# Kernel optimization log

Measured on AMD Instinct MI355X. Metric: run time of the kernel, lower is better.

The kernel has to match this reference:

```python
import jax, jax.numpy as jnp
import numpy as np

B, T, E, A = 4, 4096, 1024, 1024

def setup_inputs() -> dict:
    key = jax.random.key(0)
    k1, k2, k3, k4 = jax.random.split(key, 4)
    scale = 1.0 / np.sqrt(E)  # ~ nn.Linear default init scale
    return {
        "embedded": jax.random.normal(k1, (B, T, E), dtype=jnp.float32),
        "Wq": jax.random.uniform(k2, (A, E), jnp.float32, -scale, scale),
        "Wk": jax.random.uniform(k3, (A, E), jnp.float32, -scale, scale),
        "Wv": jax.random.uniform(k4, (A, E), jnp.float32, -scale, scale),
    }

def reference(embedded, Wq, Wk, Wv):
    # QKV projections (nn.Linear without bias: x @ W.T)
    q = jnp.einsum('bte,ae->bta', embedded, Wq)
    k = jnp.einsum('bte,ae->bta', embedded, Wk)
    v = jnp.einsum('bte,ae->bta', embedded, Wv)
    A_dim = q.shape[-1]
    # scaled scores [B, T, T]
    scores = jnp.einsum('bqa,bka->bqk', q, k) / jnp.sqrt(jnp.float32(A_dim))
    # causal mask (lower triangular allowed)
    Tq = scores.shape[-1]
    causal = jnp.tril(jnp.ones((Tq, Tq), dtype=bool))
    scores = jnp.where(causal, scores, -jnp.inf)
    probs = jax.nn.softmax(scores, axis=-1)
    out = jnp.einsum('bqk,bka->bqa', probs, v)
    return jnp.round(out, 4)
```

## Files before the change

kernel.cpp:

```cpp
#include <hip/hip_runtime.h>
#include <hip/hip_bf16.h>

using bf16 = __hip_bfloat16;

typedef __attribute__((ext_vector_type(4))) float f32x4;
typedef __attribute__((ext_vector_type(8))) short short8;

typedef const void __attribute__((address_space(1)))* gas1_t;
typedef void __attribute__((address_space(3)))* las3_t;
#define GLDS(gp, lp) __builtin_amdgcn_global_load_lds((gas1_t)(gp), (las3_t)(lp), 16, 0, 0)

__device__ inline short f2bfbits(float f) {
  union { bf16 h; short s; } u;
  u.h = __float2bfloat16(f);
  return u.s;
}
__device__ inline float bf2f(short u) {
  unsigned x = ((unsigned)(unsigned short)u) << 16;
  float f; __builtin_memcpy(&f, &x, 4); return f;
}

__device__ inline void store_out(float* C, size_t idx, float v) { C[idx] = v; }
__device__ inline void store_out(bf16* C, size_t idx, float v) { C[idx] = __float2bfloat16(v); }

template<typename TOUT, int MODE>
__global__ __launch_bounds__(512, 2) void gemm256(
    const short* __restrict__ A, int lda, size_t sAz,
    const short* __restrict__ B, int ldb, size_t sBz,
    TOUT* __restrict__ C, int ldc, size_t sCz,
    int K, float scale)
{
  int bx, by;
  if constexpr (MODE == 1) {
    const int i = blockIdx.x;
    by = (int)((__builtin_sqrtf(8.f * (float)i + 1.f) - 1.f) * 0.5f);
    if (((by * (by + 1)) >> 1) > i) by--;
    else if ((((by + 1) * (by + 2)) >> 1) <= i) by++;
    bx = i - ((by * (by + 1)) >> 1);
  } else {
    bx = blockIdx.x; by = blockIdx.y;
  }
  const int z = blockIdx.z;
  const int tri_by = (by * (by + 1)) >> 1;

  A += (size_t)z * sAz;
  B += (size_t)z * sBz;
  C += (size_t)z * sCz;

  int Klen = K;
  if (MODE == 2) Klen = min(K, (by + 1) * 256);
  const int NT = Klen >> 5;

  __shared__ short As[3][256 * 32];
  __shared__ short Bs[3][256 * 32];

  const int t = threadIdx.x;
  const int lane = t & 63;
  const int wave = t >> 6;
  const int wm = wave >> 2;
  const int wn = wave & 3;
  const int fr = lane & 15, kh = lane >> 4;
  const int koff = ((kh ^ ((fr >> 1) & 3)) << 3);

  int srow[2], scol[2];
  #pragma unroll
  for (int j = 0; j < 2; j++) {
    int e = j * 512 + t;
    srow[j] = e >> 2;
    scol[j] = (((e & 3) ^ ((e >> 3) & 3)) << 3);
  }

  f32x4 acc[8][4];
  #pragma unroll
  for (int i = 0; i < 8; i++)
    #pragma unroll
    for (int j = 0; j < 4; j++) acc[i][j] = (f32x4){0.f, 0.f, 0.f, 0.f};

  auto STAGE_A = [&](int kt) {
    const int buf = kt % 3, k0 = kt * 32;
    #pragma unroll
    for (int j = 0; j < 2; j++) {
      const short* pa;
      if constexpr (MODE == 2)
        pa = A + (size_t)(tri_by + (k0 >> 8)) * 65536 + (size_t)srow[j] * 256 + (k0 & 255) + scol[j];
      else
        pa = A + (size_t)(by * 256 + srow[j]) * lda + k0 + scol[j];
      GLDS(pa, (char*)&As[buf][0] + j * 8192 + wave * 1024);
    }
  };
  auto STAGE_B = [&](int kt) {
    const int buf = kt % 3, k0 = kt * 32;
    #pragma unroll
    for (int j = 0; j < 2; j++) {
      const short* pb = B + (size_t)(bx * 256 + srow[j]) * ldb + k0 + scol[j];
      GLDS(pb, (char*)&Bs[buf][0] + j * 8192 + wave * 1024);
    }
  };

  STAGE_A(0); STAGE_B(0);
  STAGE_A(1); STAGE_B(1);
  asm volatile("s_waitcnt vmcnt(4)\ns_barrier" ::: "memory");

  const int arow = wm * 128 + fr;
  const int brow = wn * 64 + fr;

  for (int kt = 0; kt < NT; kt++) {
    const short* as = &As[kt % 3][0];
    const short* bs = &Bs[kt % 3][0];
    short8 af[4], bfr[4];

    #pragma unroll
    for (int n = 0; n < 4; n++) bfr[n] = *(const short8*)&bs[(brow + n * 16) * 32 + koff];
    #pragma unroll
    for (int m = 0; m < 4; m++) af[m] = *(const short8*)&as[(arow + m * 16) * 32 + koff];
    if (kt + 2 < NT) STAGE_A(kt + 2);
    __builtin_amdgcn_s_barrier();
    asm volatile("s_waitcnt lgkmcnt(0)" ::: "memory");
    __builtin_amdgcn_sched_barrier(0);
    __builtin_amdgcn_s_setprio(1);
    #pragma unroll
    for (int m = 0; m < 4; m++)
      #pragma unroll
      for (int n = 0; n < 4; n++)
        acc[m][n] = __builtin_amdgcn_mfma_f32_16x16x32_bf16(af[m], bfr[n], acc[m][n], 0, 0, 0);
    __builtin_amdgcn_s_setprio(0);
    __builtin_amdgcn_sched_barrier(0);

    #pragma unroll
    for (int m = 0; m < 4; m++) af[m] = *(const short8*)&as[(arow + (m + 4) * 16) * 32 + koff];
    if (kt + 2 < NT) STAGE_B(kt + 2);
    __builtin_amdgcn_s_barrier();
    asm volatile("s_waitcnt lgkmcnt(0)" ::: "memory");
    __builtin_amdgcn_sched_barrier(0);
    __builtin_amdgcn_s_setprio(1);
    #pragma unroll
    for (int m = 0; m < 4; m++)
      #pragma unroll
      for (int n = 0; n < 4; n++)
        acc[m + 4][n] = __builtin_amdgcn_mfma_f32_16x16x32_bf16(af[m], bfr[n], acc[m + 4][n], 0, 0, 0);
    __builtin_amdgcn_s_setprio(0);
    __builtin_amdgcn_sched_barrier(0);

    if (kt + 2 < NT)      asm volatile("s_waitcnt vmcnt(4)\ns_barrier" ::: "memory");
    else if (kt + 1 < NT) asm volatile("s_waitcnt vmcnt(0)\ns_barrier" ::: "memory");
  }

  #pragma unroll
  for (int m = 0; m < 8; m++)
    #pragma unroll
    for (int n = 0; n < 4; n++) {
      int col_l = wn * 64 + n * 16 + fr;
      #pragma unroll
      for (int r = 0; r < 4; r++) {
        int row_l = wm * 128 + m * 16 + kh * 4 + r;
        if constexpr (MODE == 1)
          store_out(C, (size_t)(tri_by + bx) * 65536 + (size_t)row_l * 256 + col_l,
                    acc[m][n][r] * scale);
        else
          store_out(C, (size_t)(by * 256 + row_l) * ldc + bx * 256 + col_l,
                    acc[m][n][r] * scale);
      }
    }
}

__global__ __launch_bounds__(256) void cvt_bf16(
    const float* __restrict__ in, bf16* __restrict__ out, int n, float scale)
{
  for (int i = (blockIdx.x * 256 + threadIdx.x) * 8; i < n; i += gridDim.x * 2048) {
    f32x4 v0 = *(const f32x4*)&in[i];
    f32x4 v1 = *(const f32x4*)&in[i + 4];
    short8 o = { f2bfbits(v0[0] * scale), f2bfbits(v0[1] * scale),
                 f2bfbits(v0[2] * scale), f2bfbits(v0[3] * scale),
                 f2bfbits(v1[0] * scale), f2bfbits(v1[1] * scale),
                 f2bfbits(v1[2] * scale), f2bfbits(v1[3] * scale) };
    *(short8*)&out[i] = o;
  }
}

__global__ __launch_bounds__(256) void softmax_causal_packed(short* SP, int T)
{
  __shared__ float rowv[4096];
  __shared__ float red[4];
  const int r = blockIdx.x;
  const int z = blockIdx.y;
  const int rb = r >> 8, rl = r & 255;
  const size_t tri = (size_t)((rb * (rb + 1)) >> 1);
  short* base = SP + (size_t)z * 136 * 65536;
  const int L = r + 1;
  const int kend = (rb + 1) * 256;
  const int t = threadIdx.x;

  float lmax = -3.0e38f;
  for (int i = t * 8; i < kend; i += 2048) {
    short8 s = *(const short8*)(base + (tri + (i >> 8)) * 65536 + (size_t)rl * 256 + (i & 255));
    #pragma unroll
    for (int j = 0; j < 8; j++) {
      float v = bf2f(s[j]);
      rowv[i + j] = v;
      if (i + j < L) lmax = fmaxf(lmax, v);
    }
  }
  #pragma unroll
  for (int o = 32; o > 0; o >>= 1) lmax = fmaxf(lmax, __shfl_down(lmax, o));
  if ((t & 63) == 0) red[t >> 6] = lmax;
  __syncthreads();
  const float m = fmaxf(fmaxf(red[0], red[1]), fmaxf(red[2], red[3]));
  __syncthreads();

  float lsum = 0.f;
  for (int i = t; i < kend; i += 256) {
    float e = (i < L) ? __expf(rowv[i] - m) : 0.f;
    rowv[i] = e;
    lsum += e;
  }
  #pragma unroll
  for (int o = 32; o > 0; o >>= 1) lsum += __shfl_down(lsum, o);
  if ((t & 63) == 0) red[t >> 6] = lsum;
  __syncthreads();
  const float inv = 1.f / (red[0] + red[1] + red[2] + red[3]);

  for (int i = t * 8; i < kend; i += 2048) {
    short8 o;
    #pragma unroll
    for (int j = 0; j < 8; j++) o[j] = f2bfbits(rowv[i + j] * inv);
    *(short8*)(base + (tri + (i >> 8)) * 65536 + (size_t)rl * 256 + (i & 255)) = o;
  }
}

extern "C" void kernel_launch(void* const* d_in, const int* in_sizes, int n_in,
                              void* d_out, int out_size, void* d_ws, size_t ws_size,
                              hipStream_t stream) {
  (void)in_sizes; (void)n_in; (void)out_size; (void)ws_size;
  const float* X  = (const float*)d_in[0];
  const float* Wq = (const float*)d_in[1];
  const float* Wk = (const float*)d_in[2];
  const float* Wv = (const float*)d_in[3];
  float* Out = (float*)d_out;

  const int Bn = 4, T = 4096, E = 1024, Ad = 1024;
  const int M = Bn * T;

  char* ws = (char*)d_ws;
  short* QKb = (short*)ws;
  short* Vt  = (short*)(ws + 67108864);
  short* Xb  = (short*)(ws + 100663296);
  short* Wqk = (short*)(ws + 134217728);
  short* Wvb = (short*)(ws + 138412032);
  short* SP  = (short*)(ws + 100663296);

  dim3 blk(256), blk5(512);
  const float qscale = 0.03125f;
  const size_t SPz = (size_t)136 * 65536;

  cvt_bf16<<<dim3(8192), blk, 0, stream>>>(X, (bf16*)Xb, M * E, 1.0f);
  cvt_bf16<<<dim3(512),  blk, 0, stream>>>(Wq, (bf16*)Wqk, Ad * E, qscale);
  cvt_bf16<<<dim3(512),  blk, 0, stream>>>(Wk, (bf16*)(Wqk + (size_t)Ad * E), Ad * E, 1.0f);
  cvt_bf16<<<dim3(512),  blk, 0, stream>>>(Wv, (bf16*)Wvb, Ad * E, 1.0f);

  gemm256<bf16, 0><<<dim3(2048 / 256, M / 256), blk5, 0, stream>>>(
      Xb, E, 0, Wqk, E, 0, (bf16*)QKb, 2048, 0, E, 1.0f);
  gemm256<bf16, 0><<<dim3(M / 256, Ad / 256), blk5, 0, stream>>>(
      Wvb, E, 0, Xb, E, 0, (bf16*)Vt, M, 0, E, 1.0f);

  gemm256<bf16, 1><<<dim3(136, 1, Bn), blk5, 0, stream>>>(
      QKb, 2048, (size_t)T * 2048,
      QKb + 1024, 2048, (size_t)T * 2048,
      (bf16*)SP, 256, SPz, Ad, 1.0f);

  softmax_causal_packed<<<dim3(T, Bn), blk, 0, stream>>>(SP, T);

  gemm256<float, 2><<<dim3(Ad / 256, T / 256, Bn), blk5, 0, stream>>>(
      SP, 256, SPz,
      Vt, M, (size_t)T,
      Out, Ad, (size_t)T * Ad, T, 1.0f);
}
```

Before: 399.2 us.

## Make GEMMs persistent with XCC-local atomic tile queues and work stealing

Turns the four GEMM launches into persistent kernels. Each workgroup reads its XCC id and pulls tiles from a per-XCC atomic counter queue, stealing from other XCCs' queues once its own is empty. Tile orderings are arranged so tiles that share operands land on the same XCC for L2 reuse, and the causal PV GEMM pairs long and short rows to balance load. This adds an atomic and a barrier per tile plus a memset of the counters, and launches grids sized to fit in one wave of occupancy.

```diff
diff --git a/kernel.cpp b/kernel.cpp
--- a/kernel.cpp
+++ b/kernel.cpp
@@ -28,31 +28,17 @@
     const short* __restrict__ A, int lda, size_t sAz,
     const short* __restrict__ B, int ldb, size_t sBz,
     TOUT* __restrict__ C, int ldc, size_t sCz,
-    int K, float scale)
+    int K, float scale, int* __restrict__ qctr)
 {
-  int bx, by;
-  if constexpr (MODE == 1) {
-    const int i = blockIdx.x;
-    by = (int)((__builtin_sqrtf(8.f * (float)i + 1.f) - 1.f) * 0.5f);
-    if (((by * (by + 1)) >> 1) > i) by--;
-    else if ((((by + 1) * (by + 2)) >> 1) <= i) by++;
-    bx = i - ((by * (by + 1)) >> 1);
-  } else {
-    bx = blockIdx.x; by = blockIdx.y;
-  }
-  const int z = blockIdx.z;
-  const int tri_by = (by * (by + 1)) >> 1;
-
-  A += (size_t)z * sAz;
-  B += (size_t)z * sBz;
-  C += (size_t)z * sCz;
-
-  int Klen = K;
-  if (MODE == 2) Klen = min(K, (by + 1) * 256);
-  const int NT = Klen >> 5;
+  constexpr int QSZ = (MODE == 0) ? 64 : (MODE == 1) ? 68 : 32;
 
   __shared__ short As[3][256 * 32];
   __shared__ short Bs[3][256 * 32];
+  __shared__ int s_tile;
+
+  int xcc;
+  asm volatile("s_getreg_b32 %0, hwreg(HW_REG_XCC_ID)" : "=s"(xcc));
+  xcc &= 7;
 
   const int t = threadIdx.x;
   const int lane = t & 63;
@@ -69,98 +55,145 @@
     srow[j] = e >> 2;
     scol[j] = (((e & 3) ^ ((e >> 3) & 3)) << 3);
   }
-
-  f32x4 acc[8][4];
-  #pragma unroll
-  for (int i = 0; i < 8; i++)
-    #pragma unroll
-    for (int j = 0; j < 4; j++) acc[i][j] = (f32x4){0.f, 0.f, 0.f, 0.f};
-
-  auto STAGE_A = [&](int kt) {
-    const int buf = kt % 3, k0 = kt * 32;
-    #pragma unroll
-    for (int j = 0; j < 2; j++) {
-      const short* pa;
-      if constexpr (MODE == 2)
-        pa = A + (size_t)(tri_by + (k0 >> 8)) * 65536 + (size_t)srow[j] * 256 + (k0 & 255) + scol[j];
-      else
-        pa = A + (size_t)(by * 256 + srow[j]) * lda + k0 + scol[j];
-      GLDS(pa, (char*)&As[buf][0] + j * 8192 + wave * 1024);
-    }
-  };
-  auto STAGE_B = [&](int kt) {
-    const int buf = kt % 3, k0 = kt * 32;
-    #pragma unroll
-    for (int j = 0; j < 2; j++) {
-      const short* pb = B + (size_t)(bx * 256 + srow[j]) * ldb + k0 + scol[j];
-      GLDS(pb, (char*)&Bs[buf][0] + j * 8192 + wave * 1024);
-    }
-  };
-
-  STAGE_A(0); STAGE_B(0);
-  STAGE_A(1); STAGE_B(1);
-  asm volatile("s_waitcnt vmcnt(4)\ns_barrier" ::: "memory");
-
   const int arow = wm * 128 + fr;
   const int brow = wn * 64 + fr;
 
-  for (int kt = 0; kt < NT; kt++) {
-    const short* as = &As[kt % 3][0];
-    const short* bs = &Bs[kt % 3][0];
-    short8 af[4], bfr[4];
-
+  for (;;) {
+    if (t == 0) {
+      int tile = -1;
+      #pragma unroll
+      for (int k = 0; k < 8; k++) {
+        int q = (xcc + k) & 7;
+        int v = atomicAdd(&qctr[q], 1);
+        if (v < QSZ) { tile = q * QSZ + v; break; }
+      }
+      s_tile = tile;
+    }
+    __syncthreads();
+    const int tile = s_tile;
+    if (tile < 0) return;
+
+    int bx, by, z;
+    if constexpr (MODE == 0) {
+      const int q = tile / QSZ, v = tile % QSZ;
+      by = q * 8 + (v >> 3); bx = v & 7; z = 0;
+    } else if constexpr (MODE == 1) {
+      z = tile / 136;
+      const int r = tile % 136;
+      by = (int)((__builtin_sqrtf(8.f * (float)r + 1.f) - 1.f) * 0.5f);
+      if (((by * (by + 1)) >> 1) > r) by--;
+      else if ((((by + 1) * (by + 2)) >> 1) <= r) by++;
+      bx = r - ((by * (by + 1)) >> 1);
+    } else if constexpr (MODE == 2) {
+      z = tile >> 6;
+      const int s = tile & 63, pr = s >> 3, k = s & 7;
+      by = (k < 4) ? pr : 15 - pr;
+      bx = k & 3;
+    } else {
+      const int q = tile / QSZ, v = tile % QSZ;
+      bx = q * 8 + (v >> 2); by = v & 3; z = 0;
+    }
+    const int tri_by = (by * (by + 1)) >> 1;
+
+    const short* Az = A + (size_t)z * sAz;
+    const short* Bz = B + (size_t)z * sBz;
+    TOUT* Cz = C + (size_t)z * sCz;
+
+    int Klen = K;
+    if (MODE == 2) Klen = min(K, (by + 1) * 256);
+    const int NT = Klen >> 5;
+
+    f32x4 acc[8][4];
     #pragma unroll
-    for (int n = 0; n < 4; n++) bfr[n] = *(const short8*)&bs[(brow + n * 16) * 32 + koff];
+    for (int i = 0; i < 8; i++)
+      #pragma unroll
+      for (int j = 0; j < 4; j++) acc[i][j] = (f32x4){0.f, 0.f, 0.f, 0.f};
+
+    auto STAGE_A = [&](int kt) {
+      const int buf = kt % 3, k0 = kt * 32;
+      #pragma unroll
+      for (int j = 0; j < 2; j++) {
+        const short* pa;
+        if constexpr (MODE == 2)
+          pa = Az + (size_t)(tri_by + (k0 >> 8)) * 65536 + (size_t)srow[j] * 256 + (k0 & 255) + scol[j];
+        else
+          pa = Az + (size_t)(by * 256 + srow[j]) * lda + k0 + scol[j];
+        GLDS(pa, (char*)&As[buf][0] + j * 8192 + wave * 1024);
+      }
+    };
+    auto STAGE_B = [&](int kt) {
+      const int buf = kt % 3, k0 = kt * 32;
+      #pragma unroll
+      for (int j = 0; j < 2; j++) {
+        const short* pb = Bz + (size_t)(bx * 256 + srow[j]) * ldb + k0 + scol[j];
+        GLDS(pb, (char*)&Bs[buf][0] + j * 8192 + wave * 1024);
+      }
+    };
+
+    STAGE_A(0); STAGE_B(0);
+    STAGE_A(1); STAGE_B(1);
+    asm volatile("s_waitcnt vmcnt(4)\ns_barrier" ::: "memory");
+
+    for (int kt = 0; kt < NT; kt++) {
+      const short* as = &As[kt % 3][0];
+      const short* bs = &Bs[kt % 3][0];
+      short8 af[4], bfr[4];
+
+      #pragma unroll
+      for (int n = 0; n < 4; n++) bfr[n] = *(const short8*)&bs[(brow + n * 16) * 32 + koff];
+      #pragma unroll
+      for (int m = 0; m < 4; m++) af[m] = *(const short8*)&as[(arow + m * 16) * 32 + koff];
+      if (kt + 2 < NT) STAGE_A(kt + 2);
+      __builtin_amdgcn_s_barrier();
+      asm volatile("s_waitcnt lgkmcnt(0)" ::: "memory");
+      __builtin_amdgcn_sched_barrier(0);
+      __builtin_amdgcn_s_setprio(1);
+      #pragma unroll
+      for (int m = 0; m < 4; m++)
+        #pragma unroll
+        for (int n = 0; n < 4; n++)
+          acc[m][n] = __builtin_amdgcn_mfma_f32_16x16x32_bf16(af[m], bfr[n], acc[m][n], 0, 0, 0);
+      __builtin_amdgcn_s_setprio(0);
+      __builtin_amdgcn_sched_barrier(0);
+
+      #pragma unroll
+      for (int m = 0; m < 4; m++) af[m] = *(const short8*)&as[(arow + (m + 4) * 16) * 32 + koff];
+      if (kt + 2 < NT) STAGE_B(kt + 2);
+      __builtin_amdgcn_s_barrier();
+      asm volatile("s_waitcnt lgkmcnt(0)" ::: "memory");
+      __builtin_amdgcn_sched_barrier(0);
+      __builtin_amdgcn_s_setprio(1);
+      #pragma unroll
+      for (int m = 0; m < 4; m++)
+        #pragma unroll
+        for (int n = 0; n < 4; n++)
+          acc[m + 4][n] = __builtin_amdgcn_mfma_f32_16x16x32_bf16(af[m], bfr[n], acc[m + 4][n], 0, 0, 0);
+      __builtin_amdgcn_s_setprio(0);
+      __builtin_amdgcn_sched_barrier(0);
+
+      if (kt + 2 < NT)      asm volatile("s_waitcnt vmcnt(4)\ns_barrier" ::: "memory");
+      else if (kt + 1 < NT) asm volatile("s_waitcnt vmcnt(0)\ns_barrier" ::: "memory");
+    }
+
     #pragma unroll
-    for (int m = 0; m < 4; m++) af[m] = *(const short8*)&as[(arow + m * 16) * 32 + koff];
-    if (kt + 2 < NT) STAGE_A(kt + 2);
-    __builtin_amdgcn_s_barrier();
-    asm volatile("s_waitcnt lgkmcnt(0)" ::: "memory");
-    __builtin_amdgcn_sched_barrier(0);
-    __builtin_amdgcn_s_setprio(1);
-    #pragma unroll
-    for (int m = 0; m < 4; m++)
-      #pragma unroll
-      for (int n = 0; n < 4; n++)
-        acc[m][n] = __builtin_amdgcn_mfma_f32_16x16x32_bf16(af[m], bfr[n], acc[m][n], 0, 0, 0);
-    __builtin_amdgcn_s_setprio(0);
-    __builtin_amdgcn_sched_barrier(0);
-
-    #pragma unroll
-    for (int m = 0; m < 4; m++) af[m] = *(const short8*)&as[(arow + (m + 4) * 16) * 32 + koff];
-    if (kt + 2 < NT) STAGE_B(kt + 2);
-    __builtin_amdgcn_s_barrier();
-    asm volatile("s_waitcnt lgkmcnt(0)" ::: "memory");
-    __builtin_amdgcn_sched_barrier(0);
-    __builtin_amdgcn_s_setprio(1);
-    #pragma unroll
-    for (int m = 0; m < 4; m++)
-      #pragma unroll
-      for (int n = 0; n < 4; n++)
-        acc[m + 4][n] = __builtin_amdgcn_mfma_f32_16x16x32_bf16(af[m], bfr[n], acc[m + 4][n], 0, 0, 0);
-    __builtin_amdgcn_s_setprio(0);
-    __builtin_amdgcn_sched_barrier(0);
-
-    if (kt + 2 < NT)      asm volatile("s_waitcnt vmcnt(4)\ns_barrier" ::: "memory");
-    else if (kt + 1 < NT) asm volatile("s_waitcnt vmcnt(0)\ns_barrier" ::: "memory");
-  }
-
-  #pragma unroll
-  for (int m = 0; m < 8; m++)
-    #pragma unroll
-    for (int n = 0; n < 4; n++) {
-      int col_l = wn * 64 + n * 16 + fr;
-      #pragma unroll
-      for (int r = 0; r < 4; r++) {
-        int row_l = wm * 128 + m * 16 + kh * 4 + r;
-        if constexpr (MODE == 1)
-          store_out(C, (size_t)(tri_by + bx) * 65536 + (size_t)row_l * 256 + col_l,
-                    acc[m][n][r] * scale);
-        else
-          store_out(C, (size_t)(by * 256 + row_l) * ldc + bx * 256 + col_l,
-                    acc[m][n][r] * scale);
+    for (int m = 0; m < 8; m++)
+      #pragma unroll
+      for (int n = 0; n < 4; n++) {
+        int col_l = wn * 64 + n * 16 + fr;
+        #pragma unroll
+        for (int r = 0; r < 4; r++) {
+          int row_l = wm * 128 + m * 16 + kh * 4 + r;
+          if constexpr (MODE == 1)
+            store_out(Cz, (size_t)(tri_by + bx) * 65536 + (size_t)row_l * 256 + col_l,
+                      acc[m][n][r] * scale);
+          else
+            store_out(Cz, (size_t)(by * 256 + row_l) * ldc + bx * 256 + col_l,
+                      acc[m][n][r] * scale);
+        }
       }
-    }
+
+    __syncthreads();
+  }
 }
 
 __global__ __launch_bounds__(256) void cvt_bf16(
@@ -247,30 +280,33 @@
   short* Wqk = (short*)(ws + 134217728);
   short* Wvb = (short*)(ws + 138412032);
   short* SP  = (short*)(ws + 100663296);
+  int*  qctr = (int*)(ws + 188743680);
 
   dim3 blk(256), blk5(512);
   const float qscale = 0.03125f;
   const size_t SPz = (size_t)136 * 65536;
+
+  hipMemsetAsync(qctr, 0, 4 * 16 * sizeof(int), stream);
 
   cvt_bf16<<<dim3(8192), blk, 0, stream>>>(X, (bf16*)Xb, M * E, 1.0f);
   cvt_bf16<<<dim3(512),  blk, 0, stream>>>(Wq, (bf16*)Wqk, Ad * E, qscale);
   cvt_bf16<<<dim3(512),  blk, 0, stream>>>(Wk, (bf16*)(Wqk + (size_t)Ad * E), Ad * E, 1.0f);
   cvt_bf16<<<dim3(512),  blk, 0, stream>>>(Wv, (bf16*)Wvb, Ad * E, 1.0f);
 
-  gemm256<bf16, 0><<<dim3(2048 / 256, M / 256), blk5, 0, stream>>>(
-      Xb, E, 0, Wqk, E, 0, (bf16*)QKb, 2048, 0, E, 1.0f);
-  gemm256<bf16, 0><<<dim3(M / 256, Ad / 256), blk5, 0, stream>>>(
-      Wvb, E, 0, Xb, E, 0, (bf16*)Vt, M, 0, E, 1.0f);
-
-  gemm256<bf16, 1><<<dim3(136, 1, Bn), blk5, 0, stream>>>(
+  gemm256<bf16, 0><<<dim3(512), blk5, 0, stream>>>(
+      Xb, E, 0, Wqk, E, 0, (bf16*)QKb, 2048, 0, E, 1.0f, qctr + 0);
+  gemm256<bf16, 3><<<dim3(256), blk5, 0, stream>>>(
+      Wvb, E, 0, Xb, E, 0, (bf16*)Vt, M, 0, E, 1.0f, qctr + 16);
+
+  gemm256<bf16, 1><<<dim3(544), blk5, 0, stream>>>(
       QKb, 2048, (size_t)T * 2048,
       QKb + 1024, 2048, (size_t)T * 2048,
-      (bf16*)SP, 256, SPz, Ad, 1.0f);
+      (bf16*)SP, 256, SPz, Ad, 1.0f, qctr + 32);
 
   softmax_causal_packed<<<dim3(T, Bn), blk, 0, stream>>>(SP, T);
 
-  gemm256<float, 2><<<dim3(Ad / 256, T / 256, Bn), blk5, 0, stream>>>(
+  gemm256<float, 2><<<dim3(256), blk5, 0, stream>>>(
       SP, 256, SPz,
       Vt, M, (size_t)T,
-      Out, Ad, (size_t)T * Ad, T, 1.0f);
-}
+      Out, Ad, (size_t)T * Ad, T, 1.0f, qctr + 48);
+}
```

Measured after the change: 484.7 us. +21.4%, slower.

## Switch GEMMs to 128x256 tiles with BK=64 four-slot pipeline and balanced scheduling

Applied to the files above, without the earlier changes.

The 256x256 GEMM tile becomes a 128x256 tile, giving twice as many blocks and a 16-accumulator-per-wave footprint. The K loop now covers 64 per iteration, split into two 32-wide halves, using a four-slot LDS ring with prefetch issued between the halves. The causal PV GEMM uses a flattened grid that pairs short and long row-blocks across batches to balance triangular work, and the score GEMM maps the packed triangle onto half-height tiles. This aims at better occupancy and load balance, at the cost of more redundant B-tile loads per output and more complex index math.

```diff
diff --git a/kernel.cpp b/kernel.cpp
--- a/kernel.cpp
+++ b/kernel.cpp
@@ -24,35 +24,46 @@
 __device__ inline void store_out(bf16* C, size_t idx, float v) { C[idx] = __float2bfloat16(v); }
 
 template<typename TOUT, int MODE>
-__global__ __launch_bounds__(512, 2) void gemm256(
+__global__ __launch_bounds__(512, 2) void gemm8p(
     const short* __restrict__ A, int lda, size_t sAz,
     const short* __restrict__ B, int ldb, size_t sBz,
     TOUT* __restrict__ C, int ldc, size_t sCz,
     int K, float scale)
 {
-  int bx, by;
+  int bx, by, z;
   if constexpr (MODE == 1) {
     const int i = blockIdx.x;
-    by = (int)((__builtin_sqrtf(8.f * (float)i + 1.f) - 1.f) * 0.5f);
-    if (((by * (by + 1)) >> 1) > i) by--;
-    else if ((((by + 1) * (by + 2)) >> 1) <= i) by++;
-    bx = i - ((by * (by + 1)) >> 1);
+    int u = (int)((__builtin_sqrtf(4.f * (float)i + 1.f) - 1.f) * 0.5f);
+    while (u > 0 && u * (u + 1) > i) u--;
+    while ((u + 1) * (u + 2) <= i) u++;
+    const int rem = i - u * (u + 1);
+    if (rem < u + 1) { by = 2 * u; bx = rem; }
+    else             { by = 2 * u + 1; bx = rem - (u + 1); }
+    z = blockIdx.z;
+  } else if constexpr (MODE == 2) {
+    const int w = blockIdx.x;
+    const int k = w >> 8, c = w & 255;
+    bx = c & 3;
+    const int h = c >> 2;
+    const int byb = h & 31, zb = h >> 5;
+    by = k ? 31 - byb : byb;
+    z = zb + 2 * k;
   } else {
-    bx = blockIdx.x; by = blockIdx.y;
-  }
-  const int z = blockIdx.z;
-  const int tri_by = (by * (by + 1)) >> 1;
-
-  A += (size_t)z * sAz;
-  B += (size_t)z * sBz;
-  C += (size_t)z * sCz;
+    bx = blockIdx.x; by = blockIdx.y; z = 0;
+  }
+  const int u_rb = by >> 1;
+  const int tri_u = (u_rb * (u_rb + 1)) >> 1;
+
+  const short* Az = A + (size_t)z * sAz;
+  const short* Bz = B + (size_t)z * sBz;
+  TOUT* Cz = C + (size_t)z * sCz;
 
   int Klen = K;
-  if (MODE == 2) Klen = min(K, (by + 1) * 256);
-  const int NT = Klen >> 5;
-
-  __shared__ short As[3][256 * 32];
-  __shared__ short Bs[3][256 * 32];
+  if (MODE == 2) Klen = min(K, (u_rb + 1) * 256);
+  const int NT = Klen >> 6;
+
+  __shared__ short As[4][128 * 32];
+  __shared__ short Bs[4][256 * 32];
 
   const int t = threadIdx.x;
   const int lane = t & 63;
@@ -62,59 +73,64 @@
   const int fr = lane & 15, kh = lane >> 4;
   const int koff = ((kh ^ ((fr >> 1) & 3)) << 3);
 
-  int srow[2], scol[2];
-  #pragma unroll
-  for (int j = 0; j < 2; j++) {
-    int e = j * 512 + t;
-    srow[j] = e >> 2;
-    scol[j] = (((e & 3) ^ ((e >> 3) & 3)) << 3);
-  }
-
-  f32x4 acc[8][4];
-  #pragma unroll
-  for (int i = 0; i < 8; i++)
+  const int aro = (wm * 64 + fr) * 32;
+  const int bro = (wn * 64 + fr) * 32;
+  const int abase = by * 128;
+  const int bbase = bx * 256;
+
+  const int s_row = t >> 2;
+  const int s_sc = (((t & 3) ^ ((s_row >> 1) & 3)) << 3);
+
+  f32x4 acc[4][4];
+  #pragma unroll
+  for (int i = 0; i < 4; i++)
     #pragma unroll
     for (int j = 0; j < 4; j++) acc[i][j] = (f32x4){0.f, 0.f, 0.f, 0.f};
 
-  auto STAGE_A = [&](int kt) {
-    const int buf = kt % 3, k0 = kt * 32;
+  auto STAGE_A = [&](int kt, int ks) {
+    const int slot = (2 * kt + ks) & 3;
+    const int k0 = kt * 64 + ks * 32;
+    const short* pa;
+    if constexpr (MODE == 2)
+      pa = Az + (size_t)(tri_u + (k0 >> 8)) * 65536
+              + (size_t)((by & 1) * 128 + s_row) * 256 + (k0 & 255) + s_sc;
+    else
+      pa = Az + (size_t)(abase + s_row) * lda + k0 + s_sc;
+    GLDS(pa, (char*)&As[slot][0] + t * 16);
+  };
+  auto STAGE_B = [&](int kt, int ks) {
+    const int slot = (2 * kt + ks) & 3;
+    const int k0 = kt * 64 + ks * 32;
     #pragma unroll
     for (int j = 0; j < 2; j++) {
-      const short* pa;
-      if constexpr (MODE == 2)
-        pa = A + (size_t)(tri_by + (k0 >> 8)) * 65536 + (size_t)srow[j] * 256 + (k0 & 255) + scol[j];
-      else
-        pa = A + (size_t)(by * 256 + srow[j]) * lda + k0 + scol[j];
-      GLDS(pa, (char*)&As[buf][0] + j * 8192 + wave * 1024);
+      const int e = j * 512 + t;
+      const int row = e >> 2;
+      const int sc = (((e & 3) ^ ((row >> 1) & 3)) << 3);
+      const short* pb = Bz + (size_t)(bbase + row) * ldb + k0 + sc;
+      GLDS(pb, (char*)&Bs[slot][0] + j * 8192 + t * 16);
     }
   };
-  auto STAGE_B = [&](int kt) {
-    const int buf = kt % 3, k0 = kt * 32;
-    #pragma unroll
-    for (int j = 0; j < 2; j++) {
-      const short* pb = B + (size_t)(bx * 256 + srow[j]) * ldb + k0 + scol[j];
-      GLDS(pb, (char*)&Bs[buf][0] + j * 8192 + wave * 1024);
-    }
-  };
-
-  STAGE_A(0); STAGE_B(0);
-  STAGE_A(1); STAGE_B(1);
-  asm volatile("s_waitcnt vmcnt(4)\ns_barrier" ::: "memory");
-
-  const int arow = wm * 128 + fr;
-  const int brow = wn * 64 + fr;
+
+  STAGE_A(0, 0); STAGE_B(0, 0);
+  STAGE_A(0, 1); STAGE_B(0, 1);
+  STAGE_A(1, 0); STAGE_B(1, 0);
+  STAGE_A(1, 1); STAGE_B(1, 1);
 
   for (int kt = 0; kt < NT; kt++) {
-    const short* as = &As[kt % 3][0];
-    const short* bs = &Bs[kt % 3][0];
-    short8 af[4], bfr[4];
-
-    #pragma unroll
-    for (int n = 0; n < 4; n++) bfr[n] = *(const short8*)&bs[(brow + n * 16) * 32 + koff];
-    #pragma unroll
-    for (int m = 0; m < 4; m++) af[m] = *(const short8*)&as[(arow + m * 16) * 32 + koff];
-    if (kt + 2 < NT) STAGE_A(kt + 2);
+    const short* as0 = &As[(2 * kt) & 3][0];
+    const short* bs0 = &Bs[(2 * kt) & 3][0];
+    const short* as1 = &As[(2 * kt + 1) & 3][0];
+    const short* bs1 = &Bs[(2 * kt + 1) & 3][0];
+    short8 af[4], bf[4];
+
+    if (kt >= 1 && kt + 1 < NT) { STAGE_A(kt + 1, 1); STAGE_B(kt + 1, 1); }
+    if (kt == NT - 1) asm volatile("s_waitcnt vmcnt(0)" ::: "memory");
+    else              asm volatile("s_waitcnt vmcnt(6)" ::: "memory");
     __builtin_amdgcn_s_barrier();
+    #pragma unroll
+    for (int n = 0; n < 4; n++) bf[n] = *(const short8*)&bs0[bro + n * 512 + koff];
+    #pragma unroll
+    for (int m = 0; m < 4; m++) af[m] = *(const short8*)&as0[aro + m * 512 + koff];
     asm volatile("s_waitcnt lgkmcnt(0)" ::: "memory");
     __builtin_amdgcn_sched_barrier(0);
     __builtin_amdgcn_s_setprio(1);
@@ -122,14 +138,15 @@
     for (int m = 0; m < 4; m++)
       #pragma unroll
       for (int n = 0; n < 4; n++)
-        acc[m][n] = __builtin_amdgcn_mfma_f32_16x16x32_bf16(af[m], bfr[n], acc[m][n], 0, 0, 0);
+        acc[m][n] = __builtin_amdgcn_mfma_f32_16x16x32_bf16(af[m], bf[n], acc[m][n], 0, 0, 0);
     __builtin_amdgcn_s_setprio(0);
-    __builtin_amdgcn_sched_barrier(0);
-
-    #pragma unroll
-    for (int m = 0; m < 4; m++) af[m] = *(const short8*)&as[(arow + (m + 4) * 16) * 32 + koff];
-    if (kt + 2 < NT) STAGE_B(kt + 2);
+
     __builtin_amdgcn_s_barrier();
+    if (kt + 2 < NT) { STAGE_A(kt + 2, 0); STAGE_B(kt + 2, 0); }
+    #pragma unroll
+    for (int n = 0; n < 4; n++) bf[n] = *(const short8*)&bs1[bro + n * 512 + koff];
+    #pragma unroll
+    for (int m = 0; m < 4; m++) af[m] = *(const short8*)&as1[aro + m * 512 + koff];
     asm volatile("s_waitcnt lgkmcnt(0)" ::: "memory");
     __builtin_amdgcn_sched_barrier(0);
     __builtin_amdgcn_s_setprio(1);
@@ -137,27 +154,25 @@
     for (int m = 0; m < 4; m++)
       #pragma unroll
       for (int n = 0; n < 4; n++)
-        acc[m + 4][n] = __builtin_amdgcn_mfma_f32_16x16x32_bf16(af[m], bfr[n], acc[m + 4][n], 0, 0, 0);
+        acc[m][n] = __builtin_amdgcn_mfma_f32_16x16x32_bf16(af[m], bf[n], acc[m][n], 0, 0, 0);
     __builtin_amdgcn_s_setprio(0);
-    __builtin_amdgcn_sched_barrier(0);
-
-    if (kt + 2 < NT)      asm volatile("s_waitcnt vmcnt(4)\ns_barrier" ::: "memory");
-    else if (kt + 1 < NT) asm volatile("s_waitcnt vmcnt(0)\ns_barrier" ::: "memory");
-  }
-
-  #pragma unroll
-  for (int m = 0; m < 8; m++)
+    __builtin_amdgcn_s_barrier();
+  }
+
+  #pragma unroll
+  for (int m = 0; m < 4; m++)
     #pragma unroll
     for (int n = 0; n < 4; n++) {
       int col_l = wn * 64 + n * 16 + fr;
       #pragma unroll
       for (int r = 0; r < 4; r++) {
-        int row_l = wm * 128 + m * 16 + kh * 4 + r;
+        int row_l = wm * 64 + m * 16 + kh * 4 + r;
         if constexpr (MODE == 1)
-          store_out(C, (size_t)(tri_by + bx) * 65536 + (size_t)row_l * 256 + col_l,
+          store_out(Cz, (size_t)(tri_u + bx) * 65536
+                        + (size_t)((by & 1) * 128 + row_l) * 256 + col_l,
                     acc[m][n][r] * scale);
         else
-          store_out(C, (size_t)(by * 256 + row_l) * ldc + bx * 256 + col_l,
+          store_out(Cz, (size_t)(by * 128 + row_l) * ldc + bx * 256 + col_l,
                     acc[m][n][r] * scale);
       }
     }
@@ -257,19 +272,19 @@
   cvt_bf16<<<dim3(512),  blk, 0, stream>>>(Wk, (bf16*)(Wqk + (size_t)Ad * E), Ad * E, 1.0f);
   cvt_bf16<<<dim3(512),  blk, 0, stream>>>(Wv, (bf16*)Wvb, Ad * E, 1.0f);
 
-  gemm256<bf16, 0><<<dim3(2048 / 256, M / 256), blk5, 0, stream>>>(
+  gemm8p<bf16, 0><<<dim3(2048 / 256, M / 128), blk5, 0, stream>>>(
       Xb, E, 0, Wqk, E, 0, (bf16*)QKb, 2048, 0, E, 1.0f);
-  gemm256<bf16, 0><<<dim3(M / 256, Ad / 256), blk5, 0, stream>>>(
+  gemm8p<bf16, 0><<<dim3(M / 256, Ad / 128), blk5, 0, stream>>>(
       Wvb, E, 0, Xb, E, 0, (bf16*)Vt, M, 0, E, 1.0f);
 
-  gemm256<bf16, 1><<<dim3(136, 1, Bn), blk5, 0, stream>>>(
+  gemm8p<bf16, 1><<<dim3(272, 1, Bn), blk5, 0, stream>>>(
       QKb, 2048, (size_t)T * 2048,
       QKb + 1024, 2048, (size_t)T * 2048,
       (bf16*)SP, 256, SPz, Ad, 1.0f);
 
   softmax_causal_packed<<<dim3(T, Bn), blk, 0, stream>>>(SP, T);
 
-  gemm256<float, 2><<<dim3(Ad / 256, T / 256, Bn), blk5, 0, stream>>>(
+  gemm8p<float, 2><<<dim3(512), blk5, 0, stream>>>(
       SP, 256, SPz,
       Vt, M, (size_t)T,
       Out, Ad, (size_t)T * Ad, T, 1.0f);
```

Result: slower. 528.3 us (+32.3%).

## Restructure GEMM pipeline to 64-wide K stages and add dedicated causal PV kernel

Applied to the files above, without the earlier changes.

Changes the main 256x256 GEMM from a triple-buffered 32-wide K loop to a double-buffered 64-wide K step split into two halves. Loads are issued per half-stage across four sub-iterations, the LDS XOR swizzle is removed, and the occupancy hint of two blocks per SM is dropped. The PV product moves to a new 128x128-tile kernel with a grid ordered to balance causal work (pairing short and long row blocks) and a simple synchronous load loop. The risks are LDS bank conflicts without the swizzle, lower occupancy, and an unpipelined PV kernel.

```diff
diff --git a/kernel.cpp b/kernel.cpp
--- a/kernel.cpp
+++ b/kernel.cpp
@@ -24,7 +24,7 @@
 __device__ inline void store_out(bf16* C, size_t idx, float v) { C[idx] = __float2bfloat16(v); }
 
 template<typename TOUT, int MODE>
-__global__ __launch_bounds__(512, 2) void gemm256(
+__global__ __launch_bounds__(512) void gemm8(
     const short* __restrict__ A, int lda, size_t sAz,
     const short* __restrict__ B, int ldb, size_t sBz,
     TOUT* __restrict__ C, int ldc, size_t sCz,
@@ -47,12 +47,10 @@
   B += (size_t)z * sBz;
   C += (size_t)z * sCz;
 
-  int Klen = K;
-  if (MODE == 2) Klen = min(K, (by + 1) * 256);
-  const int NT = Klen >> 5;
-
-  __shared__ short As[3][256 * 32];
-  __shared__ short Bs[3][256 * 32];
+  const int NT = K >> 6;
+
+  __shared__ short AS[2][2][8192];
+  __shared__ short BS[2][2][8192];
 
   const int t = threadIdx.x;
   const int lane = t & 63;
@@ -60,15 +58,6 @@
   const int wm = wave >> 2;
   const int wn = wave & 3;
   const int fr = lane & 15, kh = lane >> 4;
-  const int koff = ((kh ^ ((fr >> 1) & 3)) << 3);
-
-  int srow[2], scol[2];
-  #pragma unroll
-  for (int j = 0; j < 2; j++) {
-    int e = j * 512 + t;
-    srow[j] = e >> 2;
-    scol[j] = (((e & 3) ^ ((e >> 3) & 3)) << 3);
-  }
 
   f32x4 acc[8][4];
   #pragma unroll
@@ -76,89 +65,164 @@
     #pragma unroll
     for (int j = 0; j < 4; j++) acc[i][j] = (f32x4){0.f, 0.f, 0.f, 0.f};
 
-  auto STAGE_A = [&](int kt) {
-    const int buf = kt % 3, k0 = kt * 32;
+  auto STAGE_A = [&](int tau, int h) {
+    if (tau >= NT) return;
+    const short* src = A + (size_t)(by * 256) * lda + tau * 64 + h * 32;
+    char* dst = (char*)&AS[tau & 1][h][0] + wave * 1024;
     #pragma unroll
     for (int j = 0; j < 2; j++) {
-      const short* pa;
-      if constexpr (MODE == 2)
-        pa = A + (size_t)(tri_by + (k0 >> 8)) * 65536 + (size_t)srow[j] * 256 + (k0 & 255) + scol[j];
-      else
-        pa = A + (size_t)(by * 256 + srow[j]) * lda + k0 + scol[j];
-      GLDS(pa, (char*)&As[buf][0] + j * 8192 + wave * 1024);
+      int e = j * 512 + t;
+      GLDS(src + (size_t)(e >> 2) * lda + (e & 3) * 8, dst + j * 8192);
     }
   };
-  auto STAGE_B = [&](int kt) {
-    const int buf = kt % 3, k0 = kt * 32;
+  auto STAGE_B = [&](int tau, int h) {
+    if (tau >= NT) return;
+    const short* src = B + (size_t)(bx * 256) * ldb + tau * 64 + h * 32;
+    char* dst = (char*)&BS[tau & 1][h][0] + wave * 1024;
     #pragma unroll
     for (int j = 0; j < 2; j++) {
-      const short* pb = B + (size_t)(bx * 256 + srow[j]) * ldb + k0 + scol[j];
-      GLDS(pb, (char*)&Bs[buf][0] + j * 8192 + wave * 1024);
+      int e = j * 512 + t;
+      GLDS(src + (size_t)(e >> 2) * ldb + (e & 3) * 8, dst + j * 8192);
     }
   };
 
-  STAGE_A(0); STAGE_B(0);
-  STAGE_A(1); STAGE_B(1);
-  asm volatile("s_waitcnt vmcnt(4)\ns_barrier" ::: "memory");
-
-  const int arow = wm * 128 + fr;
-  const int brow = wn * 64 + fr;
-
-  for (int kt = 0; kt < NT; kt++) {
-    const short* as = &As[kt % 3][0];
-    const short* bs = &Bs[kt % 3][0];
+  STAGE_A(0, 0); STAGE_B(0, 0);
+  STAGE_A(0, 1); STAGE_B(0, 1);
+  STAGE_A(1, 0); STAGE_B(1, 0);
+  asm volatile("s_waitcnt vmcnt(8)" ::: "memory");
+  __builtin_amdgcn_s_barrier();
+  __builtin_amdgcn_sched_barrier(0);
+
+  for (int s = 0; s < NT; s++) {
+    const int buf = s & 1;
+    #pragma unroll
+    for (int r = 0; r < 4; r++) {
+      const int kh2 = r >> 1, mh = r & 1;
+      short8 af[4], bfr[4];
+      #pragma unroll
+      for (int n = 0; n < 4; n++)
+        bfr[n] = *(const short8*)&BS[buf][kh2][(wn * 64 + n * 16 + fr) * 32 + kh * 8];
+      #pragma unroll
+      for (int m2 = 0; m2 < 4; m2++)
+        af[m2] = *(const short8*)&AS[buf][kh2][(wm * 128 + mh * 64 + m2 * 16 + fr) * 32 + kh * 8];
+
+      if      (r == 0) STAGE_A(s + 1, 1);
+      else if (r == 1) STAGE_B(s + 1, 1);
+      else if (r == 2) STAGE_A(s + 2, 0);
+      else             STAGE_B(s + 2, 0);
+
+      __builtin_amdgcn_s_barrier();
+      asm volatile("s_waitcnt lgkmcnt(0)" ::: "memory");
+      __builtin_amdgcn_sched_barrier(0);
+      __builtin_amdgcn_s_setprio(1);
+      #pragma unroll
+      for (int m2 = 0; m2 < 4; m2++)
+        #pragma unroll
+        for (int n = 0; n < 4; n++)
+          acc[mh * 4 + m2][n] =
+              __builtin_amdgcn_mfma_f32_16x16x32_bf16(af[m2], bfr[n], acc[mh * 4 + m2][n], 0, 0, 0);
+      __builtin_amdgcn_s_setprio(0);
+      __builtin_amdgcn_sched_barrier(0);
+
+      if (r == 1) {
+        if (s + 1 < NT) asm volatile("s_waitcnt vmcnt(8)" ::: "memory");
+        else            asm volatile("s_waitcnt vmcnt(0)" ::: "memory");
+      } else if (r == 3) {
+        if (s + 2 < NT) asm volatile("s_waitcnt vmcnt(8)" ::: "memory");
+        else            asm volatile("s_waitcnt vmcnt(0)" ::: "memory");
+      }
+      __builtin_amdgcn_s_barrier();
+      __builtin_amdgcn_sched_barrier(0);
+    }
+  }
+
+  #pragma unroll
+  for (int m = 0; m < 8; m++)
+    #pragma unroll
+    for (int n = 0; n < 4; n++) {
+      int col_l = wn * 64 + n * 16 + fr;
+      #pragma unroll
+      for (int r_ = 0; r_ < 4; r_++) {
+        int row_l = wm * 128 + m * 16 + kh * 4 + r_;
+        if constexpr (MODE == 1)
+          store_out(C, (size_t)(tri_by + bx) * 65536 + (size_t)row_l * 256 + col_l,
+                    acc[m][n][r_] * scale);
+        else
+          store_out(C, (size_t)(by * 256 + row_l) * ldc + bx * 256 + col_l,
+                    acc[m][n][r_] * scale);
+      }
+    }
+}
+
+__global__ __launch_bounds__(256) void gemm_pv(
+    const short* __restrict__ SP, const short* __restrict__ Vt,
+    float* __restrict__ Out)
+{
+  const int w = blockIdx.x;
+  const int c = w & 255, k = w >> 8;
+  const int bx = c & 7;
+  const int g = c >> 3;
+  const int by = (k & 1) ? 31 - g : g;
+  const int z = ((k & 1) << 1) | (k >> 1);
+
+  const int u = by >> 1;
+  const int tri_u = (u * (u + 1)) >> 1;
+  const short* A = SP + (size_t)z * 136 * 65536;
+  const int Klen = (u + 1) * 256;
+
+  __shared__ short a_lds[128 * 32];
+  __shared__ short b_lds[128 * 32];
+
+  const int t = threadIdx.x;
+  const int lane = t & 63;
+  const int wave = t >> 6;
+  const int wm = wave >> 1, wn = wave & 1;
+  const int fr = lane & 15, kh = lane >> 4;
+
+  f32x4 acc[4][4];
+  #pragma unroll
+  for (int i = 0; i < 4; i++)
+    #pragma unroll
+    for (int j = 0; j < 4; j++) acc[i][j] = (f32x4){0.f, 0.f, 0.f, 0.f};
+
+  for (int k0 = 0; k0 < Klen; k0 += 32) {
+    #pragma unroll
+    for (int i = 0; i < 2; i++) {
+      int e = i * 256 + t;
+      int r_ = e >> 2, c_ = (e & 3) * 8;
+      const short* pa = A + (size_t)(tri_u + (k0 >> 8)) * 65536
+                          + (size_t)((by & 1) * 128 + r_) * 256 + (k0 & 255) + c_;
+      const short* pb = Vt + (size_t)(bx * 128 + r_) * 16384 + z * 4096 + k0 + c_;
+      GLDS(pa, (char*)a_lds + i * 4096 + wave * 1024);
+      GLDS(pb, (char*)b_lds + i * 4096 + wave * 1024);
+    }
+    __syncthreads();
+
     short8 af[4], bfr[4];
-
-    #pragma unroll
-    for (int n = 0; n < 4; n++) bfr[n] = *(const short8*)&bs[(brow + n * 16) * 32 + koff];
-    #pragma unroll
-    for (int m = 0; m < 4; m++) af[m] = *(const short8*)&as[(arow + m * 16) * 32 + koff];
-    if (kt + 2 < NT) STAGE_A(kt + 2);
-    __builtin_amdgcn_s_barrier();
-    asm volatile("s_waitcnt lgkmcnt(0)" ::: "memory");
-    __builtin_amdgcn_sched_barrier(0);
-    __builtin_amdgcn_s_setprio(1);
+    #pragma unroll
+    for (int m = 0; m < 4; m++)
+      af[m] = *(const short8*)&a_lds[(wm * 64 + m * 16 + fr) * 32 + kh * 8];
+    #pragma unroll
+    for (int n = 0; n < 4; n++)
+      bfr[n] = *(const short8*)&b_lds[(wn * 64 + n * 16 + fr) * 32 + kh * 8];
     #pragma unroll
     for (int m = 0; m < 4; m++)
       #pragma unroll
       for (int n = 0; n < 4; n++)
         acc[m][n] = __builtin_amdgcn_mfma_f32_16x16x32_bf16(af[m], bfr[n], acc[m][n], 0, 0, 0);
-    __builtin_amdgcn_s_setprio(0);
-    __builtin_amdgcn_sched_barrier(0);
-
-    #pragma unroll
-    for (int m = 0; m < 4; m++) af[m] = *(const short8*)&as[(arow + (m + 4) * 16) * 32 + koff];
-    if (kt + 2 < NT) STAGE_B(kt + 2);
-    __builtin_amdgcn_s_barrier();
-    asm volatile("s_waitcnt lgkmcnt(0)" ::: "memory");
-    __builtin_amdgcn_sched_barrier(0);
-    __builtin_amdgcn_s_setprio(1);
-    #pragma unroll
-    for (int m = 0; m < 4; m++)
-      #pragma unroll
-      for (int n = 0; n < 4; n++)
-        acc[m + 4][n] = __builtin_amdgcn_mfma_f32_16x16x32_bf16(af[m], bfr[n], acc[m + 4][n], 0, 0, 0);
-    __builtin_amdgcn_s_setprio(0);
-    __builtin_amdgcn_sched_barrier(0);
-
-    if (kt + 2 < NT)      asm volatile("s_waitcnt vmcnt(4)\ns_barrier" ::: "memory");
-    else if (kt + 1 < NT) asm volatile("s_waitcnt vmcnt(0)\ns_barrier" ::: "memory");
-  }
-
-  #pragma unroll
-  for (int m = 0; m < 8; m++)
+    __syncthreads();
+  }
+
+  float* Cz = Out + (size_t)z * 4096 * 1024;
+  #pragma unroll
+  for (int m = 0; m < 4; m++)
     #pragma unroll
     for (int n = 0; n < 4; n++) {
       int col_l = wn * 64 + n * 16 + fr;
       #pragma unroll
-      for (int r = 0; r < 4; r++) {
-        int row_l = wm * 128 + m * 16 + kh * 4 + r;
-        if constexpr (MODE == 1)
-          store_out(C, (size_t)(tri_by + bx) * 65536 + (size_t)row_l * 256 + col_l,
-                    acc[m][n][r] * scale);
-        else
-          store_out(C, (size_t)(by * 256 + row_l) * ldc + bx * 256 + col_l,
-                    acc[m][n][r] * scale);
+      for (int r_ = 0; r_ < 4; r_++) {
+        int row_l = wm * 64 + m * 16 + kh * 4 + r_;
+        Cz[(size_t)(by * 128 + row_l) * 1024 + bx * 128 + col_l] = acc[m][n][r_];
       }
     }
 }
@@ -257,20 +321,17 @@
   cvt_bf16<<<dim3(512),  blk, 0, stream>>>(Wk, (bf16*)(Wqk + (size_t)Ad * E), Ad * E, 1.0f);
   cvt_bf16<<<dim3(512),  blk, 0, stream>>>(Wv, (bf16*)Wvb, Ad * E, 1.0f);
 
-  gemm256<bf16, 0><<<dim3(2048 / 256, M / 256), blk5, 0, stream>>>(
+  gemm8<bf16, 0><<<dim3(2048 / 256, M / 256), blk5, 0, stream>>>(
       Xb, E, 0, Wqk, E, 0, (bf16*)QKb, 2048, 0, E, 1.0f);
-  gemm256<bf16, 0><<<dim3(M / 256, Ad / 256), blk5, 0, stream>>>(
+  gemm8<bf16, 0><<<dim3(M / 256, Ad / 256), blk5, 0, stream>>>(
       Wvb, E, 0, Xb, E, 0, (bf16*)Vt, M, 0, E, 1.0f);
 
-  gemm256<bf16, 1><<<dim3(136, 1, Bn), blk5, 0, stream>>>(
+  gemm8<bf16, 1><<<dim3(136, 1, Bn), blk5, 0, stream>>>(
       QKb, 2048, (size_t)T * 2048,
       QKb + 1024, 2048, (size_t)T * 2048,
       (bf16*)SP, 256, SPz, Ad, 1.0f);
 
   softmax_causal_packed<<<dim3(T, Bn), blk, 0, stream>>>(SP, T);
 
-  gemm256<float, 2><<<dim3(Ad / 256, T / 256, Bn), blk5, 0, stream>>>(
-      SP, 256, SPz,
-      Vt, M, (size_t)T,
-      Out, Ad, (size_t)T * Ad, T, 1.0f);
-}
+  gemm_pv<<<dim3(1024), blk, 0, stream>>>(SP, Vt, Out);
+}
```

New measurement: 451.3 us. 1.13x slower.
